# Kernel tuning notes

Measured on AMD Instinct MI355X. Metric: run time of the kernel, lower is better.

Reference implementation:

```python
import jax, jax.numpy as jnp
import numpy as np

B, S, D = 2, 2048, 1024
H, HD = 16, 64  # H*HD == D (required by proj layer)
SCALE = D ** -0.5  # NOTE: original scales by full input dim (x.shape[-1]), not head dim


def setup_inputs() -> dict:
    key = jax.random.key(0)
    ks = jax.random.split(key, 7)
    std = D ** -0.5
    x = jax.random.normal(ks[0], (B, S, D), dtype=jnp.float32)
    # per-head projection weights, stacked: [H, D, HD] so x @ Wq[h] == Linear(D->HD)
    Wq = jax.random.normal(ks[1], (H, D, HD), dtype=jnp.float32) * std
    Wk = jax.random.normal(ks[2], (H, D, HD), dtype=jnp.float32) * std
    Wv = jax.random.normal(ks[3], (H, D, HD), dtype=jnp.float32) * std
    # output projection Linear(D, D) with bias
    Wp = jax.random.normal(ks[4], (D, D), dtype=jnp.float32) * std
    bp = jax.random.normal(ks[5], (D,), dtype=jnp.float32) * 0.01
    return {"x": x, "Wq": Wq, "Wk": Wk, "Wv": Wv, "Wp": Wp, "bp": bp}


def reference(x, Wq, Wk, Wv, Wp, bp):
    # All heads see the full x (atsp=False path). Dropout in eval mode (identity).
    q = jnp.einsum('bsd,hde->bhse', x, Wq)  # [B,H,S,HD]
    k = jnp.einsum('bsd,hde->bhse', x, Wk)
    v = jnp.einsum('bsd,hde->bhse', x, Wv)
    scores = jnp.einsum('bhse,bhte->bhst', q, k) * SCALE  # [B,H,S,S]
    causal = jnp.tril(jnp.ones((S, S), dtype=bool))
    scores = jnp.where(causal, scores, -jnp.inf)
    attn = jax.nn.softmax(scores, axis=-1)
    out = jnp.einsum('bhst,bhte->bhse', attn, v)          # [B,H,S,HD]
    # concat heads along last dim in head order: [B,S,H*HD]
    out = out.transpose(0, 2, 1, 3).reshape(B, S, H * HD)
    return out @ Wp.T + bp
```

## Files before the change

kernel.cpp:

```cpp
#include <hip/hip_runtime.h>

typedef __bf16 bf16x8 __attribute__((ext_vector_type(8)));
typedef __bf16 bf16x4 __attribute__((ext_vector_type(4)));
typedef float f32x4 __attribute__((ext_vector_type(4)));
typedef unsigned short u16;
typedef unsigned int u32;

static constexpr int kS = 2048, kD = 1024, kHD = 64;
static constexpr float kQScale = 0.03125f * 1.44269504f;

__device__ __forceinline__ u16 f2bf(float f) {
  union { float f; u32 u; } v; v.f = f;
  u32 r = v.u + 0x7FFFu + ((v.u >> 16) & 1u);
  return (u16)(r >> 16);
}
__device__ __forceinline__ float bf2f(u16 u) {
  union { u32 u; float f; } v; v.u = ((u32)u) << 16;
  return v.f;
}
__device__ __forceinline__ u32 pk2(float a, float b) {
  return (u32)f2bf(a) | ((u32)f2bf(b) << 16);
}
__device__ __forceinline__ f32x4 mfma16(bf16x8 a, bf16x8 b, f32x4 c) {
  return __builtin_amdgcn_mfma_f32_16x16x32_bf16(a, b, c, 0, 0, 0);
}
__device__ __forceinline__ void gld16(u16* lds, const u16* g) {
  __builtin_amdgcn_global_load_lds(
      (const __attribute__((address_space(1))) u32*)g,
      (__attribute__((address_space(3))) u32*)lds, 16, 0, 0);
}

__device__ __forceinline__ bool probe_f32(const u16* __restrict__ xr) {
  int ex = (xr[threadIdx.x] >> 7) & 0xFF;
  int n = __syncthreads_count(ex >= 134);
  return n > 8;
}

union Pack8 { u16 u[8]; uint4 v; };

__global__ void cast_all_kernel(const void* Wq, const void* Wk, const void* Wv,
                                const void* Wp, const void* x,
                                u16* __restrict__ Wt, u16* __restrict__ Wpb,
                                u16* __restrict__ xb) {
  bool f32m = probe_f32((const u16*)x);
  int bid = blockIdx.x;
  int t = threadIdx.x;
  __shared__ float Ts[64][65];
  if (bid < 768) {
    int u = bid >> 4;
    int d0 = (bid & 15) * 64;
    int w = u >> 4, h = u & 15;
    const void* srcv = (w == 0) ? Wq : (w == 1) ? Wk : Wv;
    const float* sf = (const float*)srcv + (size_t)h * kD * kHD;
    const u16*   sb = (const u16*)srcv + (size_t)h * kD * kHD;
    int row = t >> 4;
    int c4 = (t & 15) * 4;
    for (int rr = 0; rr < 64; rr += 16) {
      int r = rr + row;
      if (f32m) {
        float4 v = *(const float4*)&sf[(size_t)(d0 + r) * kHD + c4];
        Ts[r][c4 + 0] = v.x; Ts[r][c4 + 1] = v.y; Ts[r][c4 + 2] = v.z; Ts[r][c4 + 3] = v.w;
      } else {
        const u16* p = &sb[(size_t)(d0 + r) * kHD + c4];
        Ts[r][c4 + 0] = bf2f(p[0]); Ts[r][c4 + 1] = bf2f(p[1]);
        Ts[r][c4 + 2] = bf2f(p[2]); Ts[r][c4 + 3] = bf2f(p[3]);
      }
    }
    __syncthreads();
    for (int rr = 0; rr < 64; rr += 16) {
      int e = rr + row;
      uint2 pk;
      pk.x = pk2(Ts[c4 + 0][e], Ts[c4 + 1][e]);
      pk.y = pk2(Ts[c4 + 2][e], Ts[c4 + 3][e]);
      *(uint2*)&Wt[(size_t)u * (kHD * kD) + (size_t)e * kD + d0 + c4] = pk;
    }
  } else if (bid < 1792) {
    if (!f32m) return;
    int i = ((bid - 768) * 256 + t) * 4;
    float4 v = *(const float4*)((const float*)Wp + i);
    uint2 pk; pk.x = pk2(v.x, v.y); pk.y = pk2(v.z, v.w);
    *(uint2*)&Wpb[i] = pk;
  } else {
    if (!f32m) return;
    size_t i = ((size_t)(bid - 1792) * 256 + t) * 8;
    const float* xf = (const float*)x;
    float4 a = *(const float4*)&xf[i];
    float4 b = *(const float4*)&xf[i + 4];
    Pack8 pk;
    pk.u[0] = f2bf(a.x); pk.u[1] = f2bf(a.y); pk.u[2] = f2bf(a.z); pk.u[3] = f2bf(a.w);
    pk.u[4] = f2bf(b.x); pk.u[5] = f2bf(b.y); pk.u[6] = f2bf(b.z); pk.u[7] = f2bf(b.w);
    *(uint4*)&xb[i] = pk.v;
  }
}

__global__ __launch_bounds__(256) void qkv_gemm_kernel(const u16* __restrict__ xb,
    const u16* __restrict__ Wt, u16* __restrict__ Q, u16* __restrict__ K,
    u16* __restrict__ Vt, const void* __restrict__ x) {
  bool f32m = probe_f32((const u16*)x);
  const u16* xsrc = f32m ? xb : (const u16*)x;
  int m0 = blockIdx.x * 128;
  int n0 = blockIdx.y * 128;
  int w = (int)(blockIdx.y >> 3);
  const u16 *Ap, *Bp; int a0, b0;
  if (w == 2) { Ap = xsrc; a0 = m0; Bp = Wt; b0 = n0; }
  else        { Ap = Wt; a0 = n0; Bp = xsrc; b0 = m0; }
  int t = threadIdx.x;
  int wv = t >> 6, l = t & 63;
  int fr = l & 15, fq = l >> 4;
  int wI = (wv >> 1) * 64, wJ = (wv & 1) * 64;
  __shared__ __align__(16) u16 As[128][64];
  __shared__ __align__(16) u16 Bs[128][64];
  int srow = l >> 3;
  int scol = (((l & 7) ^ srow)) * 8;
  int dcol = (l & 7) * 8;
  int sw = fr & 7;
  f32x4 acc[4][4];
#pragma unroll
  for (int ii = 0; ii < 4; ++ii)
#pragma unroll
    for (int jj = 0; jj < 4; ++jj)
      for (int i = 0; i < 4; ++i) acc[ii][jj][i] = 0.f;

  for (int kb = 0; kb < kD / 64; ++kb) {
    int k0 = kb * 64;
    __syncthreads();
#pragma unroll
    for (int j = 0; j < 4; ++j) {
      int row = (wv * 4 + j) * 8 + srow;
      gld16(&As[row][dcol], &Ap[(size_t)(a0 + row) * kD + k0 + scol]);
      gld16(&Bs[row][dcol], &Bp[(size_t)(b0 + row) * kD + k0 + scol]);
    }
    __syncthreads();
    bf16x8 af[4][2], bg[4][2];
#pragma unroll
    for (int ii = 0; ii < 4; ++ii) {
      af[ii][0] = *(const bf16x8*)&As[wI + ii * 16 + fr][((0 + fq) ^ sw) * 8];
      af[ii][1] = *(const bf16x8*)&As[wI + ii * 16 + fr][((4 + fq) ^ sw) * 8];
    }
#pragma unroll
    for (int jj = 0; jj < 4; ++jj) {
      bg[jj][0] = *(const bf16x8*)&Bs[wJ + jj * 16 + fr][((0 + fq) ^ sw) * 8];
      bg[jj][1] = *(const bf16x8*)&Bs[wJ + jj * 16 + fr][((4 + fq) ^ sw) * 8];
    }
#pragma unroll
    for (int ii = 0; ii < 4; ++ii)
#pragma unroll
      for (int jj = 0; jj < 4; ++jj) {
        acc[ii][jj] = mfma16(af[ii][0], bg[jj][0], acc[ii][jj]);
        acc[ii][jj] = mfma16(af[ii][1], bg[jj][1], acc[ii][jj]);
      }
  }

  if (w == 2) {
    int uh = wv & 1;
    int u = 2 * blockIdx.y + uh;
    int h = u & 15;
#pragma unroll
    for (int jj = 0; jj < 4; ++jj) {
      int e = jj * 16 + fr;
#pragma unroll
      for (int ii = 0; ii < 4; ++ii) {
        int m = m0 + wI + ii * 16 + fq * 4;
        int b = m >> 11, s0 = m & 2047;
        int bh = b * 16 + h;
        *(bf16x4*)&Vt[((size_t)bh * kHD + e) * kS + s0] =
            __builtin_convertvector(acc[ii][jj], bf16x4);
      }
    }
  } else {
    int uh = wv >> 1;
    int u = 2 * blockIdx.y + uh;
    int h = u & 15;
    bool isQ = (w == 0);
    u16* dst = isQ ? Q : K;
#pragma unroll
    for (int jj = 0; jj < 4; ++jj) {
      int m = m0 + wJ + jj * 16 + fr;
      int b = m >> 11, s = m & 2047;
      int bh = b * 16 + h;
      size_t rowb = ((size_t)bh * kS + s) * kHD;
#pragma unroll
      for (int ii = 0; ii < 4; ++ii) {
        int e0 = ii * 16 + fq * 4;
        f32x4 v = acc[ii][jj];
        if (isQ) v *= kQScale;
        *(bf16x4*)&dst[rowb + e0] = __builtin_convertvector(v, bf16x4);
      }
    }
  }
}

static __device__ const signed char kQtab[48] = {
  15,31,30,31,
  14,29,28,30,29,
  13,27,26,28,27,
  12,25,24,26,25,
  11,23,22,24,23,
  10,21,20,22,21,
   9,19,18,20,19,
   8,17,16,18,17,
   7,16,
   6,5,4,3,2,1,0};
static __device__ const signed char kPtab[48] = {
  2,0,0,1,
  2,0,0,1,1,
  2,0,0,1,1,
  2,0,0,1,1,
  2,0,0,1,1,
  2,0,0,1,1,
  2,0,0,1,1,
  2,0,0,1,1,
  2,1,
  2,2,2,2,2,2,2};

__global__ __launch_bounds__(256) void attn_kernel(const u16* __restrict__ Q,
    const u16* __restrict__ K, const u16* __restrict__ Vt, u16* __restrict__ cat,
    float* __restrict__ Po, float* __restrict__ Pl, int split) {
  int bh = (int)(blockIdx.x & 31);
  int c  = (int)(blockIdx.x >> 5);
  int qb, part;
  if (split) { qb = kQtab[c]; part = kPtab[c]; }
  else       { qb = 31 - c;   part = 2; }
  int h0 = (qb + 2) >> 1;
  int tbeg = (part == 1) ? h0 : 0;
  int tend = (part == 0) ? h0 - 1 : qb;
  int q0 = qb * 64;
  int t = threadIdx.x;
  int wv = t >> 6, l = t & 63;
  int fr = l & 15, fq = l >> 4;
  __shared__ __align__(16) u16 Ks[2][64][64];
  __shared__ __align__(16) u16 Vs[2][64][64];
  __shared__ __align__(16) u16 Ps[4][16][64];
  const u16* Qb = Q + (size_t)bh * kS * kHD;
  const u16* Kb = K + (size_t)bh * kS * kHD;
  const u16* Vb = Vt + (size_t)bh * kHD * kS;

  int qrow = q0 + wv * 16 + fr;
  bf16x8 qf0 = *(const bf16x8*)&Qb[(size_t)qrow * kHD + fq * 8];
  bf16x8 qf1 = *(const bf16x8*)&Qb[(size_t)qrow * kHD + 32 + fq * 8];

  f32x4 O[4];
#pragma unroll
  for (int nt = 0; nt < 4; ++nt) for (int i = 0; i < 4; ++i) O[nt][i] = 0.f;
  float lsum = 0.f;

  int jr = l >> 3;
  int dcol = (l & 7) * 8;
  int scol = ((l & 7) ^ jr) * 8;
  int r0 = wv * 16 + jr;
  int r1 = r0 + 8;
  int sw = fr & 7;

  {
    int tb = tbeg * 64;
    gld16(&Ks[0][r0][dcol], &Kb[(size_t)(tb + r0) * kHD + scol]);
    gld16(&Ks[0][r1][dcol], &Kb[(size_t)(tb + r1) * kHD + scol]);
    gld16(&Vs[0][r0][dcol], &Vb[(size_t)r0 * kS + tb + scol]);
    gld16(&Vs[0][r1][dcol], &Vb[(size_t)r1 * kS + tb + scol]);
  }
  __syncthreads();

  int cur = 0;
  for (int tt = tbeg; tt <= tend; ++tt) {
    int t0 = tt * 64;
    if (tt < tend) {
      int t0n = t0 + 64;
      gld16(&Ks[cur ^ 1][r0][dcol], &Kb[(size_t)(t0n + r0) * kHD + scol]);
      gld16(&Ks[cur ^ 1][r1][dcol], &Kb[(size_t)(t0n + r1) * kHD + scol]);
      gld16(&Vs[cur ^ 1][r0][dcol], &Vb[(size_t)r0 * kS + t0n + scol]);
      gld16(&Vs[cur ^ 1][r1][dcol], &Vb[(size_t)r1 * kS + t0n + scol]);
    }
    f32x4 sc[4];
    __builtin_amdgcn_s_setprio(1);
#pragma unroll
    for (int nt = 0; nt < 4; ++nt) {
      f32x4 z; z[0] = z[1] = z[2] = z[3] = 0.f;
      bf16x8 a0 = *(const bf16x8*)&Ks[cur][nt * 16 + fr][((0 + fq) ^ sw) * 8];
      bf16x8 a1 = *(const bf16x8*)&Ks[cur][nt * 16 + fr][((4 + fq) ^ sw) * 8];
      z = mfma16(a0, qf0, z);
      z = mfma16(a1, qf1, z);
      sc[nt] = z;
    }
    __builtin_amdgcn_s_setprio(0);
    if (tt == qb) {
#pragma unroll
      for (int nt = 0; nt < 4; ++nt)
#pragma unroll
        for (int r = 0; r < 4; ++r)
          if (t0 + nt * 16 + fq * 4 + r > qrow) sc[nt][r] = -__builtin_inff();
    }
#pragma unroll
    for (int nt = 0; nt < 4; ++nt) {
#pragma unroll
      for (int r = 0; r < 4; ++r) {
        float p = exp2f(sc[nt][r]);
        sc[nt][r] = p;
        lsum += p;
      }
      *(bf16x4*)&Ps[wv][fr][(((nt * 2 + (fq >> 1)) ^ sw) * 8) + (fq & 1) * 4] =
          __builtin_convertvector(sc[nt], bf16x4);
    }
    bf16x8 pf0 = *(const bf16x8*)&Ps[wv][fr][(fq ^ sw) * 8];
    bf16x8 pf1 = *(const bf16x8*)&Ps[wv][fr][((4 + fq) ^ sw) * 8];
    __builtin_amdgcn_s_setprio(1);
#pragma unroll
    for (int nt = 0; nt < 4; ++nt) {
      bf16x8 v0 = *(const bf16x8*)&Vs[cur][nt * 16 + fr][((0 + fq) ^ sw) * 8];
      bf16x8 v1 = *(const bf16x8*)&Vs[cur][nt * 16 + fr][((4 + fq) ^ sw) * 8];
      O[nt] = mfma16(v0, pf0, O[nt]);
      O[nt] = mfma16(v1, pf1, O[nt]);
    }
    __builtin_amdgcn_s_setprio(0);
    __syncthreads();
    cur ^= 1;
  }
  lsum += __shfl_xor(lsum, 16, 64);
  lsum += __shfl_xor(lsum, 32, 64);
  if (part == 2) {
    float inv = 1.0f / lsum;
    int b = bh >> 4, h = bh & 15;
    size_t rowbase = ((size_t)(b * kS + qrow)) * kD + h * kHD;
#pragma unroll
    for (int nt = 0; nt < 4; ++nt) {
      f32x4 ov = O[nt] * inv;
      *(bf16x4*)&cat[rowbase + nt * 16 + fq * 4] = __builtin_convertvector(ov, bf16x4);
    }
  } else {
    int slot = ((bh << 4) + (qb - 16)) * 2 + part;
    float* Pb = Po + (size_t)slot * 4096 + (wv * 16 + fr) * 64;
    if (fq == 0) Pl[slot * 64 + wv * 16 + fr] = lsum;
#pragma unroll
    for (int nt = 0; nt < 4; ++nt)
      *(f32x4*)&Pb[nt * 16 + fq * 4] = O[nt];
  }
}

__global__ __launch_bounds__(256) void attn_combine_kernel(
    const float* __restrict__ Po, const float* __restrict__ Pl,
    u16* __restrict__ cat) {
  int bh = (int)(blockIdx.x >> 4);
  int lvl = (int)(blockIdx.x & 15);
  int t = threadIdx.x;
  int slot = ((bh << 4) + lvl) * 2;
  int b = bh >> 4, h = bh & 15;
  int e0 = (t & 15) * 4;
  for (int qq = 0; qq < 64; qq += 16) {
    int q = qq + (t >> 4);
    const float* A = Po + (size_t)slot * 4096 + q * 64 + e0;
    float l = Pl[slot * 64 + q] + Pl[(slot + 1) * 64 + q];
    float inv = 1.0f / l;
    f32x4 a = *(const f32x4*)A;
    f32x4 bv = *(const f32x4*)(A + 4096);
    f32x4 v = (a + bv) * inv;
    int qrow = (lvl + 16) * 64 + q;
    *(bf16x4*)&cat[((size_t)(b * kS + qrow)) * kD + h * kHD + e0] =
        __builtin_convertvector(v, bf16x4);
  }
}

__global__ __launch_bounds__(256) void out_gemm_kernel(const u16* __restrict__ cat,
    const u16* __restrict__ Wpb, const void* __restrict__ Wp,
    const void* __restrict__ bp, void* __restrict__ out,
    const void* __restrict__ x) {
  bool f32m = probe_f32((const u16*)x);
  const u16* wsrc = f32m ? Wpb : (const u16*)Wp;
  int m0 = blockIdx.x * 64;
  int n0 = blockIdx.y * 128;
  int t = threadIdx.x;
  int wv = t >> 6, l = t & 63;
  int fr = l & 15, fq = l >> 4;
  int wI = (wv >> 1) * 64, wJ = (wv & 1) * 32;
  __shared__ __align__(16) u16 As[128][64];
  __shared__ __align__(16) u16 Bs[64][64];
  int srow = l >> 3;
  int scol = (((l & 7) ^ srow)) * 8;
  int dcol = (l & 7) * 8;
  int sw = fr & 7;
  f32x4 acc[4][2];
#pragma unroll
  for (int ii = 0; ii < 4; ++ii)
#pragma unroll
    for (int jj = 0; jj < 2; ++jj)
      for (int i = 0; i < 4; ++i) acc[ii][jj][i] = 0.f;

  for (int kb = 0; kb < kD / 64; ++kb) {
    int k0 = kb * 64;
    __syncthreads();
#pragma unroll
    for (int j = 0; j < 4; ++j) {
      int row = j * 32 + wv * 8 + srow;
      gld16(&As[row][dcol], &wsrc[(size_t)(n0 + row) * kD + k0 + scol]);
    }
#pragma unroll
    for (int j = 0; j < 2; ++j) {
      int row = j * 32 + wv * 8 + srow;
      gld16(&Bs[row][dcol], &cat[(size_t)(m0 + row) * kD + k0 + scol]);
    }
    __syncthreads();
    bf16x8 af[4][2], bg[2][2];
#pragma unroll
    for (int ii = 0; ii < 4; ++ii) {
      af[ii][0] = *(const bf16x8*)&As[wI + ii * 16 + fr][((0 + fq) ^ sw) * 8];
      af[ii][1] = *(const bf16x8*)&As[wI + ii * 16 + fr][((4 + fq) ^ sw) * 8];
    }
#pragma unroll
    for (int jj = 0; jj < 2; ++jj) {
      bg[jj][0] = *(const bf16x8*)&Bs[wJ + jj * 16 + fr][((0 + fq) ^ sw) * 8];
      bg[jj][1] = *(const bf16x8*)&Bs[wJ + jj * 16 + fr][((4 + fq) ^ sw) * 8];
    }
#pragma unroll
    for (int ii = 0; ii < 4; ++ii)
#pragma unroll
      for (int jj = 0; jj < 2; ++jj) {
        acc[ii][jj] = mfma16(af[ii][0], bg[jj][0], acc[ii][jj]);
        acc[ii][jj] = mfma16(af[ii][1], bg[jj][1], acc[ii][jj]);
      }
  }
  const float* bpf = (const float*)bp;
  const u16*   bpb = (const u16*)bp;
#pragma unroll
  for (int ii = 0; ii < 4; ++ii) {
    int n = n0 + wI + ii * 16 + fq * 4;
    f32x4 bias;
    if (f32m) bias = *(const f32x4*)&bpf[n];
    else { bias[0] = bf2f(bpb[n]); bias[1] = bf2f(bpb[n + 1]);
           bias[2] = bf2f(bpb[n + 2]); bias[3] = bf2f(bpb[n + 3]); }
#pragma unroll
    for (int jj = 0; jj < 2; ++jj) {
      int m = m0 + wJ + jj * 16 + fr;
      f32x4 v = acc[ii][jj] + bias;
      if (f32m) *(f32x4*)&((float*)out)[(size_t)m * kD + n] = v;
      else      *(bf16x4*)&((u16*)out)[(size_t)m * kD + n] = __builtin_convertvector(v, bf16x4);
    }
  }
}

extern "C" void kernel_launch(void* const* d_in, const int* in_sizes, int n_in,
                              void* d_out, int out_size, void* d_ws, size_t ws_size,
                              hipStream_t stream) {
  const void* x  = d_in[0];
  const void* Wq = d_in[1];
  const void* Wk = d_in[2];
  const void* Wv = d_in[3];
  const void* Wp = d_in[4];
  const void* bp = d_in[5];

  char* ws = (char*)d_ws;
  u16* Wt  = (u16*)(ws + 256);
  u16* Wpb = (u16*)(ws + 256 + 6291456);
  u16* Qp  = (u16*)(ws + 256 + 6291456 + 2097152);
  u16* Kp  = Qp  + (size_t)32 * 2048 * 64;
  u16* Vtp = Kp  + (size_t)32 * 2048 * 64;
  u16* xb  = Vtp + (size_t)32 * 2048 * 64;
  u16* cat = xb;
  size_t poOff = 256 + 6291456 + 2097152 + (size_t)4 * 8388608;
  size_t plOff = poOff + (size_t)32 * 16 * 2 * 4096 * 4;
  size_t needWs = plOff + (size_t)32 * 16 * 2 * 64 * 4;
  int split = (ws_size >= needWs) ? 1 : 0;
  float* Po = (float*)(ws + poOff);
  float* Pl = (float*)(ws + plOff);

  cast_all_kernel<<<3840, 256, 0, stream>>>(Wq, Wk, Wv, Wp, x, Wt, Wpb, xb);
  qkv_gemm_kernel<<<dim3(32, 24), 256, 0, stream>>>(xb, Wt, Qp, Kp, Vtp, x);
  attn_kernel<<<split ? 1536 : 1024, 256, 0, stream>>>(Qp, Kp, Vtp, cat, Po, Pl, split);
  if (split)
    attn_combine_kernel<<<512, 256, 0, stream>>>(Po, Pl, cat);
  out_gemm_kernel<<<dim3(64, 8), 256, 0, stream>>>(cat, Wpb, Wp, bp, d_out, x);
}
```

Measured before the change: 179.3 us.

## Replace double-buffered K/V LDS tiles with single buffer and synchronous reload

Drops the double buffering of the K and V shared-memory tiles in the attention kernel. The next tile is now loaded only after the current tile's compute finishes, between two barriers. This halves the K/V LDS footprint, which may allow more resident blocks per CU. The cost is that global-load latency is no longer hidden behind the MFMA work of the current tile, and each iteration now has two barriers.

```diff
diff --git a/kernel.cpp b/kernel.cpp
--- a/kernel.cpp
+++ b/kernel.cpp
@@ -228,8 +228,8 @@
   int t = threadIdx.x;
   int wv = t >> 6, l = t & 63;
   int fr = l & 15, fq = l >> 4;
-  __shared__ __align__(16) u16 Ks[2][64][64];
-  __shared__ __align__(16) u16 Vs[2][64][64];
+  __shared__ __align__(16) u16 Ks[64][64];
+  __shared__ __align__(16) u16 Vs[64][64];
   __shared__ __align__(16) u16 Ps[4][16][64];
   const u16* Qb = Q + (size_t)bh * kS * kHD;
   const u16* Kb = K + (size_t)bh * kS * kHD;
@@ -253,30 +253,22 @@
 
   {
     int tb = tbeg * 64;
-    gld16(&Ks[0][r0][dcol], &Kb[(size_t)(tb + r0) * kHD + scol]);
-    gld16(&Ks[0][r1][dcol], &Kb[(size_t)(tb + r1) * kHD + scol]);
-    gld16(&Vs[0][r0][dcol], &Vb[(size_t)r0 * kS + tb + scol]);
-    gld16(&Vs[0][r1][dcol], &Vb[(size_t)r1 * kS + tb + scol]);
+    gld16(&Ks[r0][dcol], &Kb[(size_t)(tb + r0) * kHD + scol]);
+    gld16(&Ks[r1][dcol], &Kb[(size_t)(tb + r1) * kHD + scol]);
+    gld16(&Vs[r0][dcol], &Vb[(size_t)r0 * kS + tb + scol]);
+    gld16(&Vs[r1][dcol], &Vb[(size_t)r1 * kS + tb + scol]);
   }
   __syncthreads();
 
-  int cur = 0;
   for (int tt = tbeg; tt <= tend; ++tt) {
     int t0 = tt * 64;
-    if (tt < tend) {
-      int t0n = t0 + 64;
-      gld16(&Ks[cur ^ 1][r0][dcol], &Kb[(size_t)(t0n + r0) * kHD + scol]);
-      gld16(&Ks[cur ^ 1][r1][dcol], &Kb[(size_t)(t0n + r1) * kHD + scol]);
-      gld16(&Vs[cur ^ 1][r0][dcol], &Vb[(size_t)r0 * kS + t0n + scol]);
-      gld16(&Vs[cur ^ 1][r1][dcol], &Vb[(size_t)r1 * kS + t0n + scol]);
-    }
     f32x4 sc[4];
     __builtin_amdgcn_s_setprio(1);
 #pragma unroll
     for (int nt = 0; nt < 4; ++nt) {
       f32x4 z; z[0] = z[1] = z[2] = z[3] = 0.f;
-      bf16x8 a0 = *(const bf16x8*)&Ks[cur][nt * 16 + fr][((0 + fq) ^ sw) * 8];
-      bf16x8 a1 = *(const bf16x8*)&Ks[cur][nt * 16 + fr][((4 + fq) ^ sw) * 8];
+      bf16x8 a0 = *(const bf16x8*)&Ks[nt * 16 + fr][((0 + fq) ^ sw) * 8];
+      bf16x8 a1 = *(const bf16x8*)&Ks[nt * 16 + fr][((4 + fq) ^ sw) * 8];
       z = mfma16(a0, qf0, z);
       z = mfma16(a1, qf1, z);
       sc[nt] = z;
@@ -305,14 +297,21 @@
     __builtin_amdgcn_s_setprio(1);
 #pragma unroll
     for (int nt = 0; nt < 4; ++nt) {
-      bf16x8 v0 = *(const bf16x8*)&Vs[cur][nt * 16 + fr][((0 + fq) ^ sw) * 8];
-      bf16x8 v1 = *(const bf16x8*)&Vs[cur][nt * 16 + fr][((4 + fq) ^ sw) * 8];
+      bf16x8 v0 = *(const bf16x8*)&Vs[nt * 16 + fr][((0 + fq) ^ sw) * 8];
+      bf16x8 v1 = *(const bf16x8*)&Vs[nt * 16 + fr][((4 + fq) ^ sw) * 8];
       O[nt] = mfma16(v0, pf0, O[nt]);
       O[nt] = mfma16(v1, pf1, O[nt]);
     }
     __builtin_amdgcn_s_setprio(0);
-    __syncthreads();
-    cur ^= 1;
+    if (tt < tend) {
+      __syncthreads();
+      int t0n = t0 + 64;
+      gld16(&Ks[r0][dcol], &Kb[(size_t)(t0n + r0) * kHD + scol]);
+      gld16(&Ks[r1][dcol], &Kb[(size_t)(t0n + r1) * kHD + scol]);
+      gld16(&Vs[r0][dcol], &Vb[(size_t)r0 * kS + t0n + scol]);
+      gld16(&Vs[r1][dcol], &Vb[(size_t)r1 * kS + t0n + scol]);
+      __syncthreads();
+    }
   }
   lsum += __shfl_xor(lsum, 16, 64);
   lsum += __shfl_xor(lsum, 32, 64);
```

After: 181.1 us. About the same (+1.0%).
